# Performance work log

Hardware: AMD Instinct MI355X
Metric: run time of the kernel (lower is better)

## Reference

```python
import jax, jax.numpy as jnp
import numpy as np

B, L, D, H, DH = 2, 2048, 1024, 16, 64
EPS = 1e-5
ROPE_BASE = 10000.0


def _layernorm(x, w, b):
    mu = jnp.mean(x, axis=-1, keepdims=True)
    var = jnp.var(x, axis=-1, keepdims=True)
    y = (x - mu) * jax.lax.rsqrt(var + EPS)
    y = y * w
    if b is not None:
        y = y + b
    return y


def _rope(x):
    # x: [B, L, H, DH]; GPT-NeoX-style rotation over the full head dim
    inv_freq = 1.0 / (ROPE_BASE ** (jnp.arange(0, DH, 2, dtype=jnp.float32) / DH))  # [DH/2]
    t = jnp.arange(L, dtype=jnp.float32)
    freqs = jnp.outer(t, inv_freq)                       # [L, DH/2]
    cos = jnp.concatenate([jnp.cos(freqs)] * 2, axis=-1)[:, None, :]  # [L, 1, DH]
    sin = jnp.concatenate([jnp.sin(freqs)] * 2, axis=-1)[:, None, :]
    x1, x2 = jnp.split(x, 2, axis=-1)
    rot = jnp.concatenate([-x2, x1], axis=-1)
    return x * cos + rot * sin


def setup_inputs() -> dict:
    key = jax.random.key(0)
    ks = jax.random.split(key, 3)
    x = jax.random.normal(ks[0], (B, L, D), dtype=jnp.float32)
    w_qkv = jax.random.normal(ks[1], (3 * D, D), dtype=jnp.float32) * (D ** -0.5)
    w_out = jax.random.normal(ks[2], (D, D), dtype=jnp.float32) * (D ** -0.5)
    return {
        "x": x,
        "ln_w": jnp.ones((D,), jnp.float32),
        "ln_b": jnp.zeros((D,), jnp.float32),
        "w_qkv": w_qkv,
        "q_ln_w": jnp.ones((D,), jnp.float32),
        "k_ln_w": jnp.ones((D,), jnp.float32),
        "w_out": w_out,
    }


def reference(x, ln_w, ln_b, w_qkv, q_ln_w, k_ln_w, w_out):
    h = _layernorm(x, ln_w, ln_b)                         # [B, L, D]
    qkv = jnp.einsum("bld,ed->ble", h, w_qkv)            # [B, L, 3D]
    q, k, v = jnp.split(qkv, 3, axis=-1)
    q = _layernorm(q, q_ln_w, None)                       # weight-only per-token LN
    k = _layernorm(k, k_ln_w, None)
    q = _rope(q.reshape(B, L, H, DH))                     # [B, L, H, DH]
    k = _rope(k.reshape(B, L, H, DH))
    v = v.reshape(B, L, H, DH)
    ctx = jax.nn.dot_product_attention(q, k, v)           # [B, L, H, DH], scale 1/sqrt(DH)
    ctx = ctx.reshape(B, L, D)
    return jnp.einsum("bld,od->blo", ctx, w_out)
```

## Files before the change

kernel.cpp:

```cpp
#include <hip/hip_runtime.h>
#include <math.h>

#define BB 2
#define LL 2048
#define DD 1024
#define HH 16
#define DHD 64
#define NT (BB*LL)
#define D3 (3*DD)
#define D2 (2*DD)

typedef __bf16 bf16x8 __attribute__((ext_vector_type(8)));
typedef float  f32x4  __attribute__((ext_vector_type(4)));

__device__ __forceinline__ f32x4 mfma16(bf16x8 a, bf16x8 b, f32x4 c) {
    return __builtin_amdgcn_mfma_f32_16x16x32_bf16(a, b, c, 0, 0, 0);
}

__device__ __forceinline__ unsigned short f2bf(float f) {
    unsigned int u = __float_as_uint(f);
    u = (u + 0x7FFFu + ((u >> 16) & 1u)) >> 16;
    return (unsigned short)u;
}
__device__ __forceinline__ float bf2f(unsigned short s) {
    return __uint_as_float(((unsigned int)s) << 16);
}

__device__ __forceinline__ void gload16(const void* g, void* l) {
    __builtin_amdgcn_global_load_lds(
        (const __attribute__((address_space(1))) void*)g,
        (__attribute__((address_space(3))) void*)l, 16, 0, 0);
}

__device__ __forceinline__ float wred(float v) {
#pragma unroll
    for (int off = 32; off > 0; off >>= 1) v += __shfl_down(v, off, 64);
    return v;
}

__global__ __launch_bounds__(256) void cvt2_bf16(
        const float* __restrict__ s1, unsigned short* __restrict__ d1, int n1,
        const float* __restrict__ s2, unsigned short* __restrict__ d2, int n2) {
    int i = blockIdx.x * 256 + threadIdx.x;
    const float* s; unsigned short* d;
    if (i < n1) { s = s1; d = d1; }
    else { i -= n1; if (i >= n2) return; s = s2; d = d2; }
    const float4 v = ((const float4*)s)[i];
    ((ushort4*)d)[i] = make_ushort4(f2bf(v.x), f2bf(v.y), f2bf(v.z), f2bf(v.w));
}

__global__ __launch_bounds__(256) void ln_kernel(
        const float* __restrict__ x, const float* __restrict__ w,
        const float* __restrict__ b, unsigned short* __restrict__ h) {
    const int t = blockIdx.x;
    const int tid = threadIdx.x;
    const float4 v = ((const float4*)(x + (size_t)t * DD))[tid];
    float s = v.x + v.y + v.z + v.w;
    float ss = v.x*v.x + v.y*v.y + v.z*v.z + v.w*v.w;
    s = wred(s); ss = wred(ss);
    __shared__ float red[8];
    if ((tid & 63) == 0) { red[tid >> 6] = s; red[4 + (tid >> 6)] = ss; }
    __syncthreads();
    s  = red[0] + red[1] + red[2] + red[3];
    ss = red[4] + red[5] + red[6] + red[7];
    const float mu  = s * (1.0f / DD);
    const float inv = rsqrtf(ss * (1.0f / DD) - mu * mu + 1e-5f);
    const float4 wv = ((const float4*)w)[tid];
    const float4 bv = ((const float4*)b)[tid];
    *(ushort4*)(h + (size_t)t * DD + tid * 4) = make_ushort4(
        f2bf((v.x - mu) * inv * wv.x + bv.x),
        f2bf((v.y - mu) * inv * wv.y + bv.y),
        f2bf((v.z - mu) * inv * wv.z + bv.z),
        f2bf((v.w - mu) * inv * wv.w + bv.w));
}

__global__ __launch_bounds__(256) void gemm_qkv(
        const unsigned short* __restrict__ A, const unsigned short* __restrict__ B,
        unsigned short* __restrict__ qk, unsigned short* __restrict__ vt) {
    const int K = DD, N = D3;
    __shared__ unsigned short As[128 * 32];
    __shared__ unsigned short Bs[128 * 32];
    const int tid = threadIdx.x;
    const int w = tid >> 6, lane = tid & 63;
    const int l15 = lane & 15, quad = lane >> 4;
    const int wr = w >> 1, wc = w & 1;
    const int m0 = blockIdx.y << 7, n0 = blockIdx.x << 7;

    const int srow = w * 32 + (lane >> 2);
    const int skel = (lane & 3) << 3;
    const unsigned short* gA = A + (size_t)(m0 + srow) * K + skel;
    const unsigned short* gB = B + (size_t)(n0 + srow) * K + skel;
    unsigned short* lA = &As[w * 1024];
    unsigned short* lB = &Bs[w * 1024];

    f32x4 acc[4][4];
#pragma unroll
    for (int i = 0; i < 4; i++)
#pragma unroll
        for (int j = 0; j < 4; j++) acc[i][j] = (f32x4){0.f, 0.f, 0.f, 0.f};

    for (int k0 = 0; k0 < K; k0 += 32) {
        gload16(gA + k0,                 lA);
        gload16(gA + k0 + (size_t)16*K,  lA + 512);
        gload16(gB + k0,                 lB);
        gload16(gB + k0 + (size_t)16*K,  lB + 512);
        __syncthreads();
        bf16x8 af[4], bg[4];
#pragma unroll
        for (int i = 0; i < 4; i++) {
            af[i] = *(const bf16x8*)&As[(wr*64 + i*16 + l15) * 32 + quad*8];
            bg[i] = *(const bf16x8*)&Bs[(wc*64 + i*16 + l15) * 32 + quad*8];
        }
#pragma unroll
        for (int i = 0; i < 4; i++)
#pragma unroll
            for (int j = 0; j < 4; j++)
                acc[i][j] = mfma16(af[i], bg[j], acc[i][j]);
        __syncthreads();
    }
    if (n0 < D2) {
#pragma unroll
        for (int i = 0; i < 4; i++) {
            const int mrow = m0 + wr*64 + i*16 + quad*4;
#pragma unroll
            for (int j = 0; j < 4; j++) {
                const int ncol = n0 + wc*64 + j*16 + l15;
#pragma unroll
                for (int r = 0; r < 4; r++)
                    qk[(size_t)(mrow + r) * D2 + ncol] = f2bf(acc[i][j][r]);
            }
        }
    } else {
#pragma unroll
        for (int i = 0; i < 4; i++) {
            const int mrow = m0 + wr*64 + i*16 + quad*4;
            const int bb = mrow >> 11, l = mrow & (LL - 1);
#pragma unroll
            for (int j = 0; j < 4; j++) {
                const int nv = n0 + wc*64 + j*16 + l15 - D2;
                const int hh = nv >> 6, dh = nv & 63;
                *(ushort4*)&vt[((size_t)(bb*HH + hh) * DHD + dh) * LL + l] =
                    make_ushort4(f2bf(acc[i][j][0]), f2bf(acc[i][j][1]),
                                 f2bf(acc[i][j][2]), f2bf(acc[i][j][3]));
            }
        }
    }
}

__global__ __launch_bounds__(256) void gemm_out(
        const unsigned short* __restrict__ A, const unsigned short* __restrict__ B,
        float* __restrict__ C, int M, int N, int K) {
    __shared__ unsigned short As[128 * 32];
    __shared__ unsigned short Bs[128 * 32];
    const int tid = threadIdx.x;
    const int w = tid >> 6, lane = tid & 63;
    const int l15 = lane & 15, quad = lane >> 4;
    const int wr = w >> 1, wc = w & 1;
    const int m0 = blockIdx.y << 7, n0 = blockIdx.x << 7;
    const int srow = w * 32 + (lane >> 2);
    const int skel = (lane & 3) << 3;
    const unsigned short* gA = A + (size_t)(m0 + srow) * K + skel;
    const unsigned short* gB = B + (size_t)(n0 + srow) * K + skel;
    unsigned short* lA = &As[w * 1024];
    unsigned short* lB = &Bs[w * 1024];
    f32x4 acc[4][4];
#pragma unroll
    for (int i = 0; i < 4; i++)
#pragma unroll
        for (int j = 0; j < 4; j++) acc[i][j] = (f32x4){0.f, 0.f, 0.f, 0.f};
    for (int k0 = 0; k0 < K; k0 += 32) {
        gload16(gA + k0,                 lA);
        gload16(gA + k0 + (size_t)16*K,  lA + 512);
        gload16(gB + k0,                 lB);
        gload16(gB + k0 + (size_t)16*K,  lB + 512);
        __syncthreads();
        bf16x8 af[4], bg[4];
#pragma unroll
        for (int i = 0; i < 4; i++) {
            af[i] = *(const bf16x8*)&As[(wr*64 + i*16 + l15) * 32 + quad*8];
            bg[i] = *(const bf16x8*)&Bs[(wc*64 + i*16 + l15) * 32 + quad*8];
        }
#pragma unroll
        for (int i = 0; i < 4; i++)
#pragma unroll
            for (int j = 0; j < 4; j++)
                acc[i][j] = mfma16(af[i], bg[j], acc[i][j]);
        __syncthreads();
    }
#pragma unroll
    for (int i = 0; i < 4; i++) {
        const int mrow = m0 + wr*64 + i*16 + quad*4;
#pragma unroll
        for (int j = 0; j < 4; j++) {
            const int ncol = n0 + wc*64 + j*16 + l15;
#pragma unroll
            for (int r = 0; r < 4; r++)
                C[(size_t)(mrow + r) * N + ncol] = acc[i][j][r];
        }
    }
}

__global__ __launch_bounds__(256) void qk_rope_kernel(
        const unsigned short* __restrict__ qk,
        const float* __restrict__ qw, const float* __restrict__ kw,
        unsigned short* __restrict__ qarr, unsigned short* __restrict__ karr) {
    const int t = blockIdx.x;
    const int l = t & (LL - 1), b = t >> 11;
    const int tid = threadIdx.x;
    const unsigned short* base = qk + (size_t)t * D2;
    const ushort4 qu = *(const ushort4*)(base + tid * 4);
    const ushort4 ku = *(const ushort4*)(base + DD + tid * 4);
    const float q[4] = {bf2f(qu.x), bf2f(qu.y), bf2f(qu.z), bf2f(qu.w)};
    const float k[4] = {bf2f(ku.x), bf2f(ku.y), bf2f(ku.z), bf2f(ku.w)};
    float sq = q[0]+q[1]+q[2]+q[3], ssq = q[0]*q[0]+q[1]*q[1]+q[2]*q[2]+q[3]*q[3];
    float sk = k[0]+k[1]+k[2]+k[3], ssk = k[0]*k[0]+k[1]*k[1]+k[2]*k[2]+k[3]*k[3];
    sq = wred(sq); ssq = wred(ssq); sk = wred(sk); ssk = wred(ssk);
    __shared__ float red[16];
    __shared__ float qs[DD], ks[DD];
    const int wid = tid >> 6;
    if ((tid & 63) == 0) { red[wid] = sq; red[4+wid] = ssq; red[8+wid] = sk; red[12+wid] = ssk; }
    __syncthreads();
    sq = red[0]+red[1]+red[2]+red[3];    ssq = red[4]+red[5]+red[6]+red[7];
    sk = red[8]+red[9]+red[10]+red[11];  ssk = red[12]+red[13]+red[14]+red[15];
    const float muq = sq * (1.f/DD), invq = rsqrtf(ssq*(1.f/DD) - muq*muq + 1e-5f);
    const float muk = sk * (1.f/DD), invk = rsqrtf(ssk*(1.f/DD) - muk*muk + 1e-5f);
    const float4 qwv = ((const float4*)qw)[tid];
    const float4 kwv = ((const float4*)kw)[tid];
    const float qwa[4] = {qwv.x, qwv.y, qwv.z, qwv.w};
    const float kwa[4] = {kwv.x, kwv.y, kwv.z, kwv.w};
    float qn[4], kn[4];
#pragma unroll
    for (int e = 0; e < 4; e++) {
        qn[e] = (q[e] - muq) * invq * qwa[e];
        kn[e] = (k[e] - muk) * invk * kwa[e];
    }
    *(float4*)&qs[tid*4] = make_float4(qn[0], qn[1], qn[2], qn[3]);
    *(float4*)&ks[tid*4] = make_float4(kn[0], kn[1], kn[2], kn[3]);
    __syncthreads();
    const int d = tid * 4, j0 = d & 63;
    const bool first = (j0 < 32);
    const int pt = first ? (tid + 8) : (tid - 8);
    const float4 qp4 = *(const float4*)&qs[pt*4];
    const float4 kp4 = *(const float4*)&ks[pt*4];
    const float qb[4] = {qp4.x, qp4.y, qp4.z, qp4.w};
    const float kb[4] = {kp4.x, kp4.y, kp4.z, kp4.w};
    const float lf = (float)l;
    const float QS = 0.125f * 1.44269504088896340736f;
    unsigned short oq[4], ok[4];
#pragma unroll
    for (int e = 0; e < 4; e++) {
        const float fi   = (float)((j0 & 31) + e);
        const float freq = expf(fi * (-0.28782313662425576f));
        const float ang  = lf * freq;
        const float c = cosf(ang), sn = sinf(ang);
        float vq, vk;
        if (first) { vq = qn[e]*c - qb[e]*sn; vk = kn[e]*c - kb[e]*sn; }
        else       { vq = qn[e]*c + qb[e]*sn; vk = kn[e]*c + kb[e]*sn; }
        oq[e] = f2bf(vq * QS);
        ok[e] = f2bf(vk);
    }
    const int hh = tid >> 4;
    const int dh = (tid * 4) & 63;
    const size_t ro = ((size_t)(b*HH + hh) * LL + l) * DHD + dh;
    *(ushort4*)(qarr + ro) = make_ushort4(oq[0], oq[1], oq[2], oq[3]);
    *(ushort4*)(karr + ro) = make_ushort4(ok[0], ok[1], ok[2], ok[3]);
}

__global__ __launch_bounds__(256) void attn_kernel(
        const unsigned short* __restrict__ qarr,
        const unsigned short* __restrict__ karr,
        const unsigned short* __restrict__ vt,
        unsigned short* __restrict__ ctxb) {
    const int x = blockIdx.x;
    const int bh = (x & 7) + ((x >> 7) << 3);
    const int q0 = ((x >> 3) & 15) << 7;
    const int b = bh >> 4, h = bh & 15;
    const int tid = threadIdx.x, w = tid >> 6, lane = tid & 63;
    const int l15 = lane & 15, quad = lane >> 4;

    __shared__ unsigned short Ks[64 * 64];
    __shared__ unsigned short Vs[64 * 64];
    __shared__ unsigned short Pw[4][2][16][72];

    const unsigned short* kbase = karr + (size_t)bh * LL * DHD;
    const unsigned short* vbase = vt   + (size_t)bh * DHD * LL;

    bf16x8 qf[2][2];
    {
        const unsigned short* qp = qarr + ((size_t)bh*LL + q0 + w*32 + l15) * DHD + quad*8;
#pragma unroll
        for (int qt = 0; qt < 2; qt++)
#pragma unroll
            for (int c = 0; c < 2; c++)
                qf[qt][c] = *(const bf16x8*)(qp + qt*16*DHD + c*32);
    }

    const int r8 = lane >> 3, sc = lane & 7;
    float m_i[2] = {-1e30f, -1e30f};
    float l_i[2] = {0.f, 0.f};
    f32x4 o[2][4];
#pragma unroll
    for (int qt = 0; qt < 2; qt++)
#pragma unroll
        for (int nt = 0; nt < 4; nt++) o[qt][nt] = (f32x4){0.f, 0.f, 0.f, 0.f};

#pragma unroll
    for (int rd = 0; rd < 2; rd++) {
        const int row = w*8 + rd*32 + r8;
        const int chunk = sc ^ (row & 7);
        gload16(kbase + (size_t)row * DHD + chunk*8, (char*)Ks + w*1024 + rd*4096);
        gload16(vbase + (size_t)row * LL + chunk*8,  (char*)Vs + w*1024 + rd*4096);
    }

    for (int kt = 0; kt < LL/64; kt++) {
        __syncthreads();
        bf16x8 kf[4][2], vf[4][2];
#pragma unroll
        for (int t = 0; t < 4; t++)
#pragma unroll
            for (int c = 0; c < 2; c++) {
                const int slot = (quad + c*4) ^ (l15 & 7);
                kf[t][c] = *(const bf16x8*)&Ks[(t*16 + l15) * DHD + slot*8];
                vf[t][c] = *(const bf16x8*)&Vs[(t*16 + l15) * DHD + slot*8];
            }
        __syncthreads();
        if (kt + 1 < LL/64) {
#pragma unroll
            for (int rd = 0; rd < 2; rd++) {
                const int row = w*8 + rd*32 + r8;
                const int chunk = sc ^ (row & 7);
                gload16(kbase + ((size_t)((kt+1)*64 + row)) * DHD + chunk*8,
                        (char*)Ks + w*1024 + rd*4096);
                gload16(vbase + (size_t)row * LL + (kt+1)*64 + chunk*8,
                        (char*)Vs + w*1024 + rd*4096);
            }
        }

        f32x4 st[2][4];
#pragma unroll
        for (int qt = 0; qt < 2; qt++)
#pragma unroll
            for (int t = 0; t < 4; t++) {
                f32x4 z = (f32x4){0.f, 0.f, 0.f, 0.f};
                z = mfma16(kf[t][0], qf[qt][0], z);
                z = mfma16(kf[t][1], qf[qt][1], z);
                st[qt][t] = z;
            }

#pragma unroll
        for (int qt = 0; qt < 2; qt++) {
            float vmax = st[qt][0][0];
#pragma unroll
            for (int t = 0; t < 4; t++)
#pragma unroll
                for (int r = 0; r < 4; r++) vmax = fmaxf(vmax, st[qt][t][r]);
            vmax = fmaxf(vmax, __shfl_xor(vmax, 16));
            vmax = fmaxf(vmax, __shfl_xor(vmax, 32));
            const float nm = fmaxf(m_i[qt], vmax);
            const float alpha = __builtin_amdgcn_exp2f(m_i[qt] - nm);
            m_i[qt] = nm;
            float ps = 0.f;
#pragma unroll
            for (int t = 0; t < 4; t++) {
                const float p0 = __builtin_amdgcn_exp2f(st[qt][t][0] - nm);
                const float p1 = __builtin_amdgcn_exp2f(st[qt][t][1] - nm);
                const float p2 = __builtin_amdgcn_exp2f(st[qt][t][2] - nm);
                const float p3 = __builtin_amdgcn_exp2f(st[qt][t][3] - nm);
                ps += (p0 + p1) + (p2 + p3);
                *(ushort4*)&Pw[w][qt][l15][t*16 + quad*4] =
                    make_ushort4(f2bf(p0), f2bf(p1), f2bf(p2), f2bf(p3));
            }
            ps += __shfl_xor(ps, 16);
            ps += __shfl_xor(ps, 32);
            l_i[qt] = l_i[qt] * alpha + ps;
            float av[4];
#pragma unroll
            for (int r = 0; r < 4; r++) av[r] = __shfl(alpha, quad*4 + r);
            const bf16x8 ap0 = *(const bf16x8*)&Pw[w][qt][l15][quad*8];
            const bf16x8 ap1 = *(const bf16x8*)&Pw[w][qt][l15][32 + quad*8];
#pragma unroll
            for (int nt = 0; nt < 4; nt++) {
                f32x4 t0 = o[qt][nt];
                t0[0] *= av[0]; t0[1] *= av[1]; t0[2] *= av[2]; t0[3] *= av[3];
                t0 = mfma16(ap0, vf[nt][0], t0);
                t0 = mfma16(ap1, vf[nt][1], t0);
                o[qt][nt] = t0;
            }
        }
    }

#pragma unroll
    for (int qt = 0; qt < 2; qt++) {
        float lv[4];
#pragma unroll
        for (int r = 0; r < 4; r++) lv[r] = __shfl(l_i[qt], quad*4 + r);
#pragma unroll
        for (int r = 0; r < 4; r++) {
            const float inv = 1.f / lv[r];
            const size_t row = (size_t)(b*LL + q0 + w*32 + qt*16 + quad*4 + r);
#pragma unroll
            for (int nt = 0; nt < 4; nt++)
                ctxb[row * DD + h*DHD + nt*16 + l15] = f2bf(o[qt][nt][r] * inv);
        }
    }
}

extern "C" void kernel_launch(void* const* d_in, const int* in_sizes, int n_in,
                              void* d_out, int out_size, void* d_ws, size_t ws_size,
                              hipStream_t stream) {
    const float* x      = (const float*)d_in[0];
    const float* ln_w   = (const float*)d_in[1];
    const float* ln_b   = (const float*)d_in[2];
    const float* w_qkv  = (const float*)d_in[3];
    const float* q_ln_w = (const float*)d_in[4];
    const float* k_ln_w = (const float*)d_in[5];
    const float* w_out  = (const float*)d_in[6];
    float* out = (float*)d_out;

    char* ws = (char*)d_ws;
    unsigned short* hb   = (unsigned short*)ws;
    unsigned short* karr = (unsigned short*)ws;
    unsigned short* qk   = (unsigned short*)(ws + ((size_t)8  << 20));
    unsigned short* ctxb = (unsigned short*)(ws + ((size_t)8  << 20));
    unsigned short* vtp  = (unsigned short*)(ws + ((size_t)24 << 20));
    unsigned short* qarr = (unsigned short*)(ws + ((size_t)32 << 20));
    unsigned short* wqb  = (unsigned short*)(ws + ((size_t)40 << 20));
    unsigned short* wob  = (unsigned short*)(ws + ((size_t)46 << 20));

    cvt2_bf16<<<4096, 256, 0, stream>>>(w_qkv, wqb, 786432, w_out, wob, 262144);
    ln_kernel<<<NT, 256, 0, stream>>>(x, ln_w, ln_b, hb);
    gemm_qkv<<<dim3(D3/128, NT/128), 256, 0, stream>>>(hb, wqb, qk, vtp);
    qk_rope_kernel<<<NT, 256, 0, stream>>>(qk, q_ln_w, k_ln_w, qarr, karr);
    attn_kernel<<<512, 256, 0, stream>>>(qarr, karr, vtp, ctxb);
    gemm_out<<<dim3(DD/128, NT/128), 256, 0, stream>>>(ctxb, wob, out, NT, DD, DD);
}
```

Before: 243.7 us.

## Split-KV attention with fixed-offset softmax, MFMA row sums, and fused LN/convert

Attention now splits the KV sequence in two, launching twice as many blocks. Each block writes unnormalised bf16 partial outputs and row sums, and a new combine kernel adds the halves and normalises. The online-softmax max tracking and rescaling are replaced by a constant -64 offset folded into the MFMA accumulator init. This relies on layer-normed Q/K keeping scores bounded, and could overflow exp2 for extreme inputs or non-unit LN weights. Row sums are computed by an MFMA against a ones vector, bf16 packing uses a cheaper perm, and the weight-conversion kernel is merged into the LayerNorm launch.

```diff
diff --git a/kernel.cpp b/kernel.cpp
--- a/kernel.cpp
+++ b/kernel.cpp
@@ -38,23 +38,29 @@
     return v;
 }
 
-__global__ __launch_bounds__(256) void cvt2_bf16(
-        const float* __restrict__ s1, unsigned short* __restrict__ d1, int n1,
-        const float* __restrict__ s2, unsigned short* __restrict__ d2, int n2) {
-    int i = blockIdx.x * 256 + threadIdx.x;
-    const float* s; unsigned short* d;
-    if (i < n1) { s = s1; d = d1; }
-    else { i -= n1; if (i >= n2) return; s = s2; d = d2; }
-    const float4 v = ((const float4*)s)[i];
-    ((ushort4*)d)[i] = make_ushort4(f2bf(v.x), f2bf(v.y), f2bf(v.z), f2bf(v.w));
-}
-
-__global__ __launch_bounds__(256) void ln_kernel(
+__device__ __forceinline__ unsigned int pack_bf2(float p0, float p1) {
+    const unsigned int u0 = __float_as_uint(p0) + 0x8000u;
+    const unsigned int u1 = __float_as_uint(p1) + 0x8000u;
+    return __builtin_amdgcn_perm(u1, u0, 0x07060302u);
+}
+
+__global__ __launch_bounds__(256) void ln_cvt_kernel(
         const float* __restrict__ x, const float* __restrict__ w,
-        const float* __restrict__ b, unsigned short* __restrict__ h) {
-    const int t = blockIdx.x;
+        const float* __restrict__ b, unsigned short* __restrict__ h,
+        const float* __restrict__ wq, unsigned short* __restrict__ wqb,
+        const float* __restrict__ wo, unsigned short* __restrict__ wob) {
+    const int bx = blockIdx.x;
     const int tid = threadIdx.x;
-    const float4 v = ((const float4*)(x + (size_t)t * DD))[tid];
+    if (bx >= NT) {
+        int i = (bx - NT) * 256 + tid;
+        const float* s; unsigned short* d;
+        if (i < 786432) { s = wq; d = wqb; }
+        else            { i -= 786432; s = wo; d = wob; }
+        const float4 v = ((const float4*)s)[i];
+        ((ushort4*)d)[i] = make_ushort4(f2bf(v.x), f2bf(v.y), f2bf(v.z), f2bf(v.w));
+        return;
+    }
+    const float4 v = ((const float4*)(x + (size_t)bx * DD))[tid];
     float s = v.x + v.y + v.z + v.w;
     float ss = v.x*v.x + v.y*v.y + v.z*v.z + v.w*v.w;
     s = wred(s); ss = wred(ss);
@@ -67,7 +73,7 @@
     const float inv = rsqrtf(ss * (1.0f / DD) - mu * mu + 1e-5f);
     const float4 wv = ((const float4*)w)[tid];
     const float4 bv = ((const float4*)b)[tid];
-    *(ushort4*)(h + (size_t)t * DD + tid * 4) = make_ushort4(
+    *(ushort4*)(h + (size_t)bx * DD + tid * 4) = make_ushort4(
         f2bf((v.x - mu) * inv * wv.x + bv.x),
         f2bf((v.y - mu) * inv * wv.y + bv.y),
         f2bf((v.z - mu) * inv * wv.z + bv.z),
@@ -77,7 +83,7 @@
 __global__ __launch_bounds__(256) void gemm_qkv(
         const unsigned short* __restrict__ A, const unsigned short* __restrict__ B,
         unsigned short* __restrict__ qk, unsigned short* __restrict__ vt) {
-    const int K = DD, N = D3;
+    const int K = DD;
     __shared__ unsigned short As[128 * 32];
     __shared__ unsigned short Bs[128 * 32];
     const int tid = threadIdx.x;
@@ -266,15 +272,19 @@
     *(ushort4*)(karr + ro) = make_ushort4(ok[0], ok[1], ok[2], ok[3]);
 }
 
-__global__ __launch_bounds__(256) void attn_kernel(
+__global__ __launch_bounds__(256, 4) void attn_kernel(
         const unsigned short* __restrict__ qarr,
         const unsigned short* __restrict__ karr,
         const unsigned short* __restrict__ vt,
-        unsigned short* __restrict__ ctxb) {
+        unsigned short* __restrict__ opart,
+        float* __restrict__ lpart) {
     const int x = blockIdx.x;
-    const int bh = (x & 7) + ((x >> 7) << 3);
-    const int q0 = ((x >> 3) & 15) << 7;
+    const int g  = (x & 7) | ((x >> 7) << 3);
+    const int qblk = (x >> 3) & 15;
+    const int s = g & 1, bh = g >> 1;
     const int b = bh >> 4, h = bh & 15;
+    const int q0 = qblk << 7;
+    const int kvbase = s << 10;
     const int tid = threadIdx.x, w = tid >> 6, lane = tid & 63;
     const int l15 = lane & 15, quad = lane >> 4;
 
@@ -282,8 +292,8 @@
     __shared__ unsigned short Vs[64 * 64];
     __shared__ unsigned short Pw[4][2][16][72];
 
-    const unsigned short* kbase = karr + (size_t)bh * LL * DHD;
-    const unsigned short* vbase = vt   + (size_t)bh * DHD * LL;
+    const unsigned short* kbase = karr + ((size_t)bh * LL + kvbase) * DHD;
+    const unsigned short* vbase = vt   + (size_t)bh * DHD * LL + kvbase;
 
     bf16x8 qf[2][2];
     {
@@ -295,14 +305,18 @@
                 qf[qt][c] = *(const bf16x8*)(qp + qt*16*DHD + c*32);
     }
 
+    bf16x8 ones;
+#pragma unroll
+    for (int i = 0; i < 8; i++) ones[i] = (__bf16)1.0f;
+
     const int r8 = lane >> 3, sc = lane & 7;
-    float m_i[2] = {-1e30f, -1e30f};
-    float l_i[2] = {0.f, 0.f};
-    f32x4 o[2][4];
-#pragma unroll
-    for (int qt = 0; qt < 2; qt++)
+    f32x4 o[2][4], lacc[2];
+#pragma unroll
+    for (int qt = 0; qt < 2; qt++) {
+        lacc[qt] = (f32x4){0.f, 0.f, 0.f, 0.f};
 #pragma unroll
         for (int nt = 0; nt < 4; nt++) o[qt][nt] = (f32x4){0.f, 0.f, 0.f, 0.f};
+    }
 
 #pragma unroll
     for (int rd = 0; rd < 2; rd++) {
@@ -312,7 +326,7 @@
         gload16(vbase + (size_t)row * LL + chunk*8,  (char*)Vs + w*1024 + rd*4096);
     }
 
-    for (int kt = 0; kt < LL/64; kt++) {
+    for (int kt = 0; kt < 16; kt++) {
         __syncthreads();
         bf16x8 kf[4][2], vf[4][2];
 #pragma unroll
@@ -324,7 +338,7 @@
                 vf[t][c] = *(const bf16x8*)&Vs[(t*16 + l15) * DHD + slot*8];
             }
         __syncthreads();
-        if (kt + 1 < LL/64) {
+        if (kt + 1 < 16) {
 #pragma unroll
             for (int rd = 0; rd < 2; rd++) {
                 const int row = w*8 + rd*32 + r8;
@@ -336,52 +350,34 @@
             }
         }
 
-        f32x4 st[2][4];
-#pragma unroll
-        for (int qt = 0; qt < 2; qt++)
+#pragma unroll
+        for (int qt = 0; qt < 2; qt++) {
+            f32x4 st[4];
 #pragma unroll
             for (int t = 0; t < 4; t++) {
-                f32x4 z = (f32x4){0.f, 0.f, 0.f, 0.f};
+                f32x4 z = (f32x4){-64.f, -64.f, -64.f, -64.f};
                 z = mfma16(kf[t][0], qf[qt][0], z);
                 z = mfma16(kf[t][1], qf[qt][1], z);
-                st[qt][t] = z;
-            }
-
-#pragma unroll
-        for (int qt = 0; qt < 2; qt++) {
-            float vmax = st[qt][0][0];
-#pragma unroll
-            for (int t = 0; t < 4; t++)
-#pragma unroll
-                for (int r = 0; r < 4; r++) vmax = fmaxf(vmax, st[qt][t][r]);
-            vmax = fmaxf(vmax, __shfl_xor(vmax, 16));
-            vmax = fmaxf(vmax, __shfl_xor(vmax, 32));
-            const float nm = fmaxf(m_i[qt], vmax);
-            const float alpha = __builtin_amdgcn_exp2f(m_i[qt] - nm);
-            m_i[qt] = nm;
-            float ps = 0.f;
+                st[t] = z;
+            }
 #pragma unroll
             for (int t = 0; t < 4; t++) {
-                const float p0 = __builtin_amdgcn_exp2f(st[qt][t][0] - nm);
-                const float p1 = __builtin_amdgcn_exp2f(st[qt][t][1] - nm);
-                const float p2 = __builtin_amdgcn_exp2f(st[qt][t][2] - nm);
-                const float p3 = __builtin_amdgcn_exp2f(st[qt][t][3] - nm);
-                ps += (p0 + p1) + (p2 + p3);
-                *(ushort4*)&Pw[w][qt][l15][t*16 + quad*4] =
-                    make_ushort4(f2bf(p0), f2bf(p1), f2bf(p2), f2bf(p3));
-            }
-            ps += __shfl_xor(ps, 16);
-            ps += __shfl_xor(ps, 32);
-            l_i[qt] = l_i[qt] * alpha + ps;
-            float av[4];
-#pragma unroll
-            for (int r = 0; r < 4; r++) av[r] = __shfl(alpha, quad*4 + r);
+                const float p0 = __builtin_amdgcn_exp2f(st[t][0]);
+                const float p1 = __builtin_amdgcn_exp2f(st[t][1]);
+                const float p2 = __builtin_amdgcn_exp2f(st[t][2]);
+                const float p3 = __builtin_amdgcn_exp2f(st[t][3]);
+                uint2 pk;
+                pk.x = pack_bf2(p0, p1);
+                pk.y = pack_bf2(p2, p3);
+                *(uint2*)&Pw[w][qt][l15][t*16 + quad*4] = pk;
+            }
             const bf16x8 ap0 = *(const bf16x8*)&Pw[w][qt][l15][quad*8];
             const bf16x8 ap1 = *(const bf16x8*)&Pw[w][qt][l15][32 + quad*8];
+            lacc[qt] = mfma16(ap0, ones, lacc[qt]);
+            lacc[qt] = mfma16(ap1, ones, lacc[qt]);
 #pragma unroll
             for (int nt = 0; nt < 4; nt++) {
                 f32x4 t0 = o[qt][nt];
-                t0[0] *= av[0]; t0[1] *= av[1]; t0[2] *= av[2]; t0[3] *= av[3];
                 t0 = mfma16(ap0, vf[nt][0], t0);
                 t0 = mfma16(ap1, vf[nt][1], t0);
                 o[qt][nt] = t0;
@@ -389,20 +385,44 @@
         }
     }
 
+    unsigned short* op = opart + (size_t)s * NT * DD;
 #pragma unroll
     for (int qt = 0; qt < 2; qt++) {
-        float lv[4];
-#pragma unroll
-        for (int r = 0; r < 4; r++) lv[r] = __shfl(l_i[qt], quad*4 + r);
 #pragma unroll
         for (int r = 0; r < 4; r++) {
-            const float inv = 1.f / lv[r];
-            const size_t row = (size_t)(b*LL + q0 + w*32 + qt*16 + quad*4 + r);
+            const int qrow = q0 + w*32 + qt*16 + quad*4 + r;
+            const size_t token = (size_t)b * LL + qrow;
 #pragma unroll
             for (int nt = 0; nt < 4; nt++)
-                ctxb[row * DD + h*DHD + nt*16 + l15] = f2bf(o[qt][nt][r] * inv);
-        }
-    }
+                op[token * DD + h*DHD + nt*16 + l15] = f2bf(o[qt][nt][r]);
+        }
+        if (l15 == 0) {
+#pragma unroll
+            for (int r = 0; r < 4; r++)
+                lpart[((size_t)s * BB*HH + bh) * LL + q0 + w*32 + qt*16 + quad*4 + r] =
+                    lacc[qt][r];
+        }
+    }
+}
+
+__global__ __launch_bounds__(256) void combine_kernel(
+        const unsigned short* __restrict__ opart, const float* __restrict__ lpart,
+        unsigned short* __restrict__ ctx) {
+    const int token = blockIdx.x;
+    const int tid = threadIdx.x;
+    const int b = token >> 11, l = token & (LL - 1);
+    const int h = tid >> 4;
+    const size_t idx = (size_t)token * DD + tid * 4;
+    const ushort4 a = *(const ushort4*)(opart + idx);
+    const ushort4 c = *(const ushort4*)(opart + (size_t)NT * DD + idx);
+    const float l1 = lpart[((size_t)(b*HH + h)) * LL + l];
+    const float l2 = lpart[((size_t)BB*HH*LL) + ((size_t)(b*HH + h)) * LL + l];
+    const float inv = 1.0f / (l1 + l2);
+    *(ushort4*)(ctx + idx) = make_ushort4(
+        f2bf((bf2f(a.x) + bf2f(c.x)) * inv),
+        f2bf((bf2f(a.y) + bf2f(c.y)) * inv),
+        f2bf((bf2f(a.z) + bf2f(c.z)) * inv),
+        f2bf((bf2f(a.w) + bf2f(c.w)) * inv));
 }
 
 extern "C" void kernel_launch(void* const* d_in, const int* in_sizes, int n_in,
@@ -418,19 +438,22 @@
     float* out = (float*)d_out;
 
     char* ws = (char*)d_ws;
-    unsigned short* hb   = (unsigned short*)ws;
-    unsigned short* karr = (unsigned short*)ws;
-    unsigned short* qk   = (unsigned short*)(ws + ((size_t)8  << 20));
-    unsigned short* ctxb = (unsigned short*)(ws + ((size_t)8  << 20));
-    unsigned short* vtp  = (unsigned short*)(ws + ((size_t)24 << 20));
-    unsigned short* qarr = (unsigned short*)(ws + ((size_t)32 << 20));
-    unsigned short* wqb  = (unsigned short*)(ws + ((size_t)40 << 20));
-    unsigned short* wob  = (unsigned short*)(ws + ((size_t)46 << 20));
-
-    cvt2_bf16<<<4096, 256, 0, stream>>>(w_qkv, wqb, 786432, w_out, wob, 262144);
-    ln_kernel<<<NT, 256, 0, stream>>>(x, ln_w, ln_b, hb);
+    unsigned short* hb    = (unsigned short*)ws;
+    unsigned short* karr  = (unsigned short*)ws;
+    unsigned short* ctxb  = (unsigned short*)ws;
+    unsigned short* qk    = (unsigned short*)(ws + ((size_t)8  << 20));
+    unsigned short* opart = (unsigned short*)(ws + ((size_t)8  << 20));
+    unsigned short* vtp   = (unsigned short*)(ws + ((size_t)24 << 20));
+    unsigned short* qarr  = (unsigned short*)(ws + ((size_t)32 << 20));
+    unsigned short* wqb   = (unsigned short*)(ws + ((size_t)40 << 20));
+    float*          lpart = (float*)(ws + ((size_t)40 << 20));
+    unsigned short* wob   = (unsigned short*)(ws + ((size_t)46 << 20));
+
+    ln_cvt_kernel<<<NT + 4096, 256, 0, stream>>>(x, ln_w, ln_b, hb,
+                                                 w_qkv, wqb, w_out, wob);
     gemm_qkv<<<dim3(D3/128, NT/128), 256, 0, stream>>>(hb, wqb, qk, vtp);
     qk_rope_kernel<<<NT, 256, 0, stream>>>(qk, q_ln_w, k_ln_w, qarr, karr);
-    attn_kernel<<<512, 256, 0, stream>>>(qarr, karr, vtp, ctxb);
+    attn_kernel<<<1024, 256, 0, stream>>>(qarr, karr, vtp, opart, lpart);
+    combine_kernel<<<NT, 256, 0, stream>>>(opart, lpart, ctxb);
     gemm_out<<<dim3(DD/128, NT/128), 256, 0, stream>>>(ctxb, wob, out, NT, DD, DD);
 }
```

Measured after the change: 245.8 us. No clear change (+0.8%).
